# Kernel optimization log

Measured on AMD Instinct MI355X. Metric: run time of the kernel, lower is better.

Reference implementation:

```python
import jax, jax.numpy as jnp
import numpy as np

INPUT_DIM = 512
D_KQ = 64
D_V = 64
SEQ = 8192


def setup_inputs() -> dict:
    key = jax.random.key(0)
    k_x, k_q, k_k, k_v = jax.random.split(key, 4)
    x = jax.random.normal(k_x, (SEQ, INPUT_DIM), dtype=jnp.float32)
    # Original uses torch.rand (uniform [0,1)) for the parameters.
    W_query = jax.random.uniform(k_q, (INPUT_DIM, D_KQ), dtype=jnp.float32)
    W_key = jax.random.uniform(k_k, (INPUT_DIM, D_KQ), dtype=jnp.float32)
    W_value = jax.random.uniform(k_v, (INPUT_DIM, D_V), dtype=jnp.float32)
    return {"x": x, "W_query": W_query, "W_key": W_key, "W_value": W_value}


def reference(x, W_query, W_key, W_value):
    # Full-recompute path of AttentionOptimized: single-head attention.
    Q = x @ W_query          # [T, d_kq]
    K = x @ W_key            # [T, d_kq]
    V = x @ W_value          # [T, d_v]
    scale = jnp.asarray(D_KQ, x.dtype) ** 0.5
    scores = Q @ K.T         # [T, T]
    attn = jax.nn.softmax(scores / scale, axis=-1)
    return attn @ V          # [T, d_v]
```

## Files before the change

### kernel.cpp

```cpp
#include <hip/hip_runtime.h>
#include <hip/hip_bf16.h>
#include <math.h>

#define SEQ 8192
#define DIN 512
#define DH  64
#define SG  8
#define CHUNK (SEQ / SG)
#define BK  64
#define NIT (CHUNK / BK)
#define LDP 72
#define SXP 516

typedef float f32x4 __attribute__((ext_vector_type(4)));
typedef short short8 __attribute__((ext_vector_type(8)));
typedef ushort us4 __attribute__((ext_vector_type(4)));

static __device__ __forceinline__ ushort bf16_of(float v) {
  __hip_bfloat16 h = __float2bfloat16(v);
  return *reinterpret_cast<ushort*>(&h);
}
static __device__ __forceinline__ float f_of_bf16(ushort u) {
  __hip_bfloat16 h;
  *reinterpret_cast<ushort*>(&h) = u;
  return __bfloat162float(h);
}
static __device__ __forceinline__ f32x4 mfma16(short8 a, short8 b, f32x4 c) {
  return __builtin_amdgcn_mfma_f32_16x16x32_bf16(a, b, c, 0, 0, 0);
}
static __device__ __forceinline__ uint pack_bf16(float a, float b) {
  __hip_bfloat162 h2 = __float22bfloat162_rn(make_float2(a, b));
  return *reinterpret_cast<uint*>(&h2);
}

__global__ __launch_bounds__(256) void prep_kernel(
    const float* __restrict__ Wq, const float* __restrict__ Wk,
    const float* __restrict__ Wv, ushort* __restrict__ Wth,
    ushort* __restrict__ Wtl) {
  __shared__ float sw[64][65];
  const int mat = blockIdx.x >> 3;
  const int kc  = blockIdx.x & 7;
  const float* W = (mat == 0) ? Wq : ((mat == 1) ? Wk : Wv);
  const float scale = (mat == 0) ? 0.125f * 1.44269504088896f : 1.0f;
  const int tid = threadIdx.x;
#pragma unroll
  for (int j = 0; j < 16; ++j) {
    const int i = tid + 256 * j;
    sw[i >> 6][i & 63] =
        W[(size_t)(kc * 64 + (i >> 6)) * 64 + (i & 63)] * scale;
  }
  __syncthreads();
  const int n  = tid >> 2;
  const int ks = (tid & 3) * 16;
  ushort hb[16] __attribute__((aligned(16)));
  ushort lb[16] __attribute__((aligned(16)));
#pragma unroll
  for (int j = 0; j < 16; ++j) {
    const float w = sw[ks + j][n];
    const ushort h = bf16_of(w);
    hb[j] = h;
    lb[j] = bf16_of(w - f_of_bf16(h));
  }
  const size_t base = (size_t)mat * 64 * 512 + (size_t)n * 512 + kc * 64 + ks;
  *reinterpret_cast<short8*>(Wth + base)     = *reinterpret_cast<short8*>(hb);
  *reinterpret_cast<short8*>(Wth + base + 8) = *reinterpret_cast<short8*>(hb + 8);
  *reinterpret_cast<short8*>(Wtl + base)     = *reinterpret_cast<short8*>(lb);
  *reinterpret_cast<short8*>(Wtl + base + 8) = *reinterpret_cast<short8*>(lb + 8);
}

__global__ __launch_bounds__(256, 2) void pgemm_kernel(
    const float* __restrict__ x, const ushort* __restrict__ Wth,
    const ushort* __restrict__ Wtl,
    ushort* __restrict__ Qh, ushort* __restrict__ Ql,
    ushort* __restrict__ Kh, ushort* __restrict__ Kl,
    ushort* __restrict__ Vt) {
  __shared__ float sx[16][SXP];
  float* mb = &sx[0][0];

  const int tid = threadIdx.x;
  const int wv = tid >> 6, lane = tid & 63;
  const int ln = lane & 15, qd = lane >> 4;
  const int rb = blockIdx.x * 16;

  {
    const float4* xg = reinterpret_cast<const float4*>(x + (size_t)rb * DIN);
#pragma unroll
    for (int j = 0; j < 8; ++j) {
      const int idx = tid + 256 * j;
      const int row = idx >> 7;
      const int col = (idx & 127) * 4;
      *reinterpret_cast<float4*>(&sx[row][col]) = xg[idx];
    }
  }
  __syncthreads();

  f32x4 acc[3][4];
#pragma unroll
  for (int m = 0; m < 3; ++m)
#pragma unroll
    for (int nt = 0; nt < 4; ++nt)
#pragma unroll
      for (int i = 0; i < 4; ++i) acc[m][nt][i] = 0.f;

  const int kb = wv * 128;

  short8 wb[2][8];
#define LDG(kt_, m_, buf_)                                                     \
  do {                                                                         \
    const int k0_ = kb + (kt_) * 32;                                           \
    const ushort* Wh_ = Wth + (size_t)(m_) * 64 * 512;                         \
    const ushort* Wl_ = Wtl + (size_t)(m_) * 64 * 512;                         \
    _Pragma("unroll") for (int nt = 0; nt < 4; ++nt) {                         \
      const size_t wo = (size_t)(nt * 16 + ln) * 512 + k0_ + qd * 8;           \
      wb[buf_][nt * 2]     = *reinterpret_cast<const short8*>(Wh_ + wo);       \
      wb[buf_][nt * 2 + 1] = *reinterpret_cast<const short8*>(Wl_ + wo);       \
    }                                                                          \
  } while (0)

  LDG(0, 0, 0);
#pragma unroll
  for (int kt = 0; kt < 4; ++kt) {
    const int k0 = kb + kt * 32;
    float xs[8];
    *reinterpret_cast<float4*>(xs) =
        *reinterpret_cast<const float4*>(&sx[ln][k0 + qd * 8]);
    *reinterpret_cast<float4*>(xs + 4) =
        *reinterpret_cast<const float4*>(&sx[ln][k0 + qd * 8 + 4]);
    ushort ah[8] __attribute__((aligned(16)));
    ushort al[8] __attribute__((aligned(16)));
#pragma unroll
    for (int j = 0; j < 8; ++j) {
      const ushort h = bf16_of(xs[j]);
      ah[j] = h;
      al[j] = bf16_of(xs[j] - f_of_bf16(h));
    }
    const short8 Ah = *reinterpret_cast<short8*>(ah);
    const short8 Al = *reinterpret_cast<short8*>(al);
#pragma unroll
    for (int m = 0; m < 3; ++m) {
      const int g = kt * 3 + m;
      const int buf = g & 1;
      if (g < 11) {
        const int gn = g + 1;
        LDG(gn / 3, gn % 3, buf ^ 1);
      }
#pragma unroll
      for (int nt = 0; nt < 4; ++nt) {
        acc[m][nt] = mfma16(Ah, wb[buf][nt * 2],     acc[m][nt]);
        acc[m][nt] = mfma16(Ah, wb[buf][nt * 2 + 1], acc[m][nt]);
        acc[m][nt] = mfma16(Al, wb[buf][nt * 2],     acc[m][nt]);
      }
    }
  }
#undef LDG

  const int eidx = (qd * 4) * 64 + ln;
  __syncthreads();
  if (wv >= 2) {
    float* b = mb + (size_t)(wv - 2) * 3072;
#pragma unroll
    for (int m = 0; m < 3; ++m)
#pragma unroll
      for (int nt = 0; nt < 4; ++nt)
#pragma unroll
        for (int r = 0; r < 4; ++r)
          b[m * 1024 + eidx + r * 64 + nt * 16] = acc[m][nt][r];
  }
  __syncthreads();
  if (wv < 2) {
    const float* b = mb + (size_t)wv * 3072;
#pragma unroll
    for (int m = 0; m < 3; ++m)
#pragma unroll
      for (int nt = 0; nt < 4; ++nt)
#pragma unroll
        for (int r = 0; r < 4; ++r)
          acc[m][nt][r] += b[m * 1024 + eidx + r * 64 + nt * 16];
  }
  __syncthreads();
  if (wv == 1) {
#pragma unroll
    for (int m = 0; m < 3; ++m)
#pragma unroll
      for (int nt = 0; nt < 4; ++nt)
#pragma unroll
        for (int r = 0; r < 4; ++r)
          mb[m * 1024 + eidx + r * 64 + nt * 16] = acc[m][nt][r];
  }
  __syncthreads();
  if (wv == 0) {
#pragma unroll
    for (int m = 0; m < 3; ++m)
#pragma unroll
      for (int nt = 0; nt < 4; ++nt)
#pragma unroll
        for (int r = 0; r < 4; ++r)
          acc[m][nt][r] += mb[m * 1024 + eidx + r * 64 + nt * 16];

#pragma unroll
    for (int m = 0; m < 2; ++m) {
      ushort* H = (m == 0) ? Qh : Kh;
      ushort* L = (m == 0) ? Ql : Kl;
#pragma unroll
      for (int nt = 0; nt < 4; ++nt)
#pragma unroll
        for (int r = 0; r < 4; ++r) {
          const float v = acc[m][nt][r];
          const int row = rb + qd * 4 + r;
          const int col = nt * 16 + ln;
          const ushort h = bf16_of(v);
          H[(size_t)row * DH + col] = h;
          L[(size_t)row * DH + col] = bf16_of(v - f_of_bf16(h));
        }
    }
#pragma unroll
    for (int nt = 0; nt < 4; ++nt) {
      ushort vp[4] __attribute__((aligned(8)));
#pragma unroll
      for (int r = 0; r < 4; ++r) vp[r] = bf16_of(acc[2][nt][r]);
      *reinterpret_cast<us4*>(Vt + (size_t)(nt * 16 + ln) * SEQ + rb + qd * 4) =
          *reinterpret_cast<us4*>(vp);
    }
  }
}

__global__ __launch_bounds__(256, 2) void flash_kernel(
    const ushort* __restrict__ Qh, const ushort* __restrict__ Ql,
    const ushort* __restrict__ Kh, const ushort* __restrict__ Kl,
    const ushort* __restrict__ Vt,
    ushort* __restrict__ Opart, float* __restrict__ Mpart,
    float* __restrict__ Lpart) {
  __shared__ __attribute__((aligned(16))) ushort sKh[BK][LDP];
  __shared__ __attribute__((aligned(16))) ushort sKl[BK][LDP];
  __shared__ __attribute__((aligned(16))) ushort sVt[DH][LDP];

  const int tid  = threadIdx.x;
  const int wv   = tid >> 6;
  const int lane = tid & 63;
  const int ln   = lane & 15;
  const int qd   = lane >> 4;
  const int bid  = blockIdx.x;
  const int sg   = bid & 7;
  const int qt   = bid >> 3;
  const int qrow0  = qt * 128 + wv * 32;
  const int k0base = sg * CHUNK;

  const int r0 = tid >> 3, g0 = (tid & 7) * 8;
  const int r1 = r0 + 32,  g1 = g0;

  const int sA = ((qd & 1) * 2) * 16 + ln;
  const int sB = sA + 16;
  const bool hiQd = (qd >= 2);

  const ushort one_u = (ln == 0) ? (ushort)0x3F80 : (ushort)0;
  short8 afr1;
#pragma unroll
  for (int j = 0; j < 8; ++j) afr1[j] = (short)one_u;

  short8 bqh[2][2], bql[2][2];
#pragma unroll
  for (int s = 0; s < 2; ++s)
#pragma unroll
    for (int kt = 0; kt < 2; ++kt) {
      bqh[s][kt] = *reinterpret_cast<const short8*>(
          Qh + (size_t)(qrow0 + s * 16 + ln) * DH + kt * 32 + qd * 8);
      bql[s][kt] = *reinterpret_cast<const short8*>(
          Ql + (size_t)(qrow0 + s * 16 + ln) * DH + kt * 32 + qd * 8);
    }

  f32x4 accO[2][4], accL[2];
  float m_run[2] = {-INFINITY, -INFINITY};
#pragma unroll
  for (int s = 0; s < 2; ++s) {
#pragma unroll
    for (int nt = 0; nt < 4; ++nt)
#pragma unroll
      for (int i = 0; i < 4; ++i) accO[s][nt][i] = 0.f;
#pragma unroll
    for (int i = 0; i < 4; ++i) accL[s][i] = 0.f;
  }

  uint4 pk0, pk1, pl0, pl1, pv0, pv1;
#define LOAD_TILES(k0_)                                                        \
  do {                                                                         \
    pk0 = *reinterpret_cast<const uint4*>(Kh + (size_t)((k0_) + r0) * DH + g0);\
    pk1 = *reinterpret_cast<const uint4*>(Kh + (size_t)((k0_) + r1) * DH + g1);\
    pl0 = *reinterpret_cast<const uint4*>(Kl + (size_t)((k0_) + r0) * DH + g0);\
    pl1 = *reinterpret_cast<const uint4*>(Kl + (size_t)((k0_) + r1) * DH + g1);\
    pv0 = *reinterpret_cast<const uint4*>(Vt + (size_t)r0 * SEQ + (k0_) + g0); \
    pv1 = *reinterpret_cast<const uint4*>(Vt + (size_t)r1 * SEQ + (k0_) + g1); \
  } while (0)

  LOAD_TILES(k0base);

  for (int it = 0; it < NIT; ++it) {
    *reinterpret_cast<uint4*>(&sKh[r0][g0]) = pk0;
    *reinterpret_cast<uint4*>(&sKh[r1][g1]) = pk1;
    *reinterpret_cast<uint4*>(&sKl[r0][g0]) = pl0;
    *reinterpret_cast<uint4*>(&sKl[r1][g1]) = pl1;
    *reinterpret_cast<uint4*>(&sVt[r0][g0]) = pv0;
    *reinterpret_cast<uint4*>(&sVt[r1][g1]) = pv1;
    __syncthreads();

    const int k0n = k0base + ((it + 1 < NIT) ? (it + 1) : (NIT - 1)) * BK;
    LOAD_TILES(k0n);

    f32x4 accS[2][4];
#pragma unroll
    for (int nt = 0; nt < 4; ++nt) {
#pragma unroll
      for (int s = 0; s < 2; ++s)
#pragma unroll
        for (int i = 0; i < 4; ++i) accS[s][nt][i] = 0.f;
      const short8 kh0 = *reinterpret_cast<const short8*>(&sKh[nt * 16 + ln][qd * 8]);
      const short8 kh1 = *reinterpret_cast<const short8*>(&sKh[nt * 16 + ln][32 + qd * 8]);
      const short8 kl0 = *reinterpret_cast<const short8*>(&sKl[nt * 16 + ln][qd * 8]);
      const short8 kl1 = *reinterpret_cast<const short8*>(&sKl[nt * 16 + ln][32 + qd * 8]);
#pragma unroll
      for (int s = 0; s < 2; ++s) {
        accS[s][nt] = mfma16(kh0, bqh[s][0], accS[s][nt]);
        accS[s][nt] = mfma16(kh1, bqh[s][1], accS[s][nt]);
        accS[s][nt] = mfma16(kh0, bql[s][0], accS[s][nt]);
        accS[s][nt] = mfma16(kh1, bql[s][1], accS[s][nt]);
        accS[s][nt] = mfma16(kl0, bqh[s][0], accS[s][nt]);
        accS[s][nt] = mfma16(kl1, bqh[s][1], accS[s][nt]);
      }
    }

    uint pkd[2][4][2];
#pragma unroll
    for (int s = 0; s < 2; ++s) {
      float tmax = fmaxf(
          fmaxf(fmaxf(accS[s][0][0], accS[s][0][1]), fmaxf(accS[s][0][2], accS[s][0][3])),
          fmaxf(fmaxf(accS[s][1][0], accS[s][1][1]), fmaxf(accS[s][1][2], accS[s][1][3])));
      tmax = fmaxf(tmax, fmaxf(
          fmaxf(fmaxf(accS[s][2][0], accS[s][2][1]), fmaxf(accS[s][2][2], accS[s][2][3])),
          fmaxf(fmaxf(accS[s][3][0], accS[s][3][1]), fmaxf(accS[s][3][2], accS[s][3][3]))));
      tmax = fmaxf(tmax, __shfl_xor(tmax, 16));
      tmax = fmaxf(tmax, __shfl_xor(tmax, 32));
      const float mnew  = fmaxf(m_run[s], tmax);
      const float alpha = exp2f(m_run[s] - mnew);
      m_run[s] = mnew;
#pragma unroll
      for (int nt = 0; nt < 4; ++nt) {
        const float p0 = exp2f(accS[s][nt][0] - mnew);
        const float p1 = exp2f(accS[s][nt][1] - mnew);
        const float p2 = exp2f(accS[s][nt][2] - mnew);
        const float p3 = exp2f(accS[s][nt][3] - mnew);
        pkd[s][nt][0] = pack_bf16(p0, p1);
        pkd[s][nt][1] = pack_bf16(p2, p3);
#pragma unroll
        for (int i = 0; i < 4; ++i) accO[s][nt][i] *= alpha;
      }
      accL[s][0] *= alpha;
    }

#pragma unroll
    for (int kt2 = 0; kt2 < 2; ++kt2) {
      short8 pfrag[2];
#pragma unroll
      for (int s = 0; s < 2; ++s) {
        const uint pA0 = pkd[s][kt2 * 2][0],     pA1 = pkd[s][kt2 * 2][1];
        const uint pB0 = pkd[s][kt2 * 2 + 1][0], pB1 = pkd[s][kt2 * 2 + 1][1];
        uint4 du;
        const uint xA = (uint)__shfl((int)pA0, sA);
        const uint xB = (uint)__shfl((int)pB0, sA);
        du.x = hiQd ? xB : xA;
        const uint yA = (uint)__shfl((int)pA1, sA);
        const uint yB = (uint)__shfl((int)pB1, sA);
        du.y = hiQd ? yB : yA;
        const uint zA = (uint)__shfl((int)pA0, sB);
        const uint zB = (uint)__shfl((int)pB0, sB);
        du.z = hiQd ? zB : zA;
        const uint wA = (uint)__shfl((int)pA1, sB);
        const uint wB = (uint)__shfl((int)pB1, sB);
        du.w = hiQd ? wB : wA;
        pfrag[s] = *reinterpret_cast<short8*>(&du);
      }
#pragma unroll
      for (int nt2 = 0; nt2 < 4; ++nt2) {
        const short8 vA = *reinterpret_cast<const short8*>(
            &sVt[nt2 * 16 + ln][kt2 * 32 + qd * 8]);
        accO[0][nt2] = mfma16(vA, pfrag[0], accO[0][nt2]);
        accO[1][nt2] = mfma16(vA, pfrag[1], accO[1][nt2]);
      }
      accL[0] = mfma16(afr1, pfrag[0], accL[0]);
      accL[1] = mfma16(afr1, pfrag[1], accL[1]);
    }
    __syncthreads();
  }
#undef LOAD_TILES

#pragma unroll
  for (int s = 0; s < 2; ++s) {
    const int qrow = qrow0 + s * 16 + ln;
    ushort* Ob = Opart + ((size_t)sg * SEQ + qrow) * DH;
#pragma unroll
    for (int nt = 0; nt < 4; ++nt) {
      ushort op[4] __attribute__((aligned(8)));
#pragma unroll
      for (int r = 0; r < 4; ++r) op[r] = bf16_of(accO[s][nt][r]);
      *reinterpret_cast<us4*>(Ob + nt * 16 + qd * 4) =
          *reinterpret_cast<us4*>(op);
    }
    if (qd == 0) {
      Mpart[(size_t)sg * SEQ + qrow] = m_run[s];
      Lpart[(size_t)sg * SEQ + qrow] = accL[s][0];
    }
  }
}

__global__ __launch_bounds__(256) void merge_kernel(
    const ushort* __restrict__ Opart, const float* __restrict__ Mpart,
    const float* __restrict__ Lpart, float* __restrict__ out) {
  const int idx = blockIdx.x * 256 + threadIdx.x;
  const int row = idx >> 4;
  const int c4  = (idx & 15) * 4;

  float m[SG];
  float M = -INFINITY;
#pragma unroll
  for (int i = 0; i < SG; ++i) {
    m[i] = Mpart[(size_t)i * SEQ + row];
    M = fmaxf(M, m[i]);
  }
  float L = 0.f;
  float a0 = 0.f, a1 = 0.f, a2 = 0.f, a3 = 0.f;
#pragma unroll
  for (int i = 0; i < SG; ++i) {
    const float w = exp2f(m[i] - M);
    L += w * Lpart[(size_t)i * SEQ + row];
    const us4 o = *reinterpret_cast<const us4*>(
        Opart + ((size_t)i * SEQ + row) * DH + c4);
    a0 += w * f_of_bf16(o[0]);
    a1 += w * f_of_bf16(o[1]);
    a2 += w * f_of_bf16(o[2]);
    a3 += w * f_of_bf16(o[3]);
  }
  const float rL = 1.0f / L;
  float4 res = make_float4(a0 * rL, a1 * rL, a2 * rL, a3 * rL);
  *reinterpret_cast<float4*>(out + (size_t)row * DH + c4) = res;
}

extern "C" void kernel_launch(void* const* d_in, const int* in_sizes, int n_in,
                              void* d_out, int out_size, void* d_ws, size_t ws_size,
                              hipStream_t stream) {
  const float* x  = (const float*)d_in[0];
  const float* Wq = (const float*)d_in[1];
  const float* Wk = (const float*)d_in[2];
  const float* Wv = (const float*)d_in[3];
  float* out = (float*)d_out;

  const size_t S64 = (size_t)SEQ * DH;
  ushort* Qh = (ushort*)d_ws;
  ushort* Ql = Qh + S64;
  ushort* Kh = Ql + S64;
  ushort* Kl = Kh + S64;
  ushort* Vt = Kl + S64;
  ushort* Op = Vt + S64;
  ushort* Wth = Op;
  ushort* Wtl = Wth + (size_t)3 * 64 * 512;
  float*  Mp = (float*)(Op + (size_t)SG * S64);
  float*  Lp = Mp + (size_t)SG * SEQ;

  prep_kernel<<<24, 256, 0, stream>>>(Wq, Wk, Wv, Wth, Wtl);
  pgemm_kernel<<<SEQ / 16, 256, 0, stream>>>(x, Wth, Wtl, Qh, Ql, Kh, Kl, Vt);
  flash_kernel<<<(SEQ / 128) * SG, 256, 0, stream>>>(Qh, Ql, Kh, Kl, Vt, Op, Mp, Lp);
  merge_kernel<<<(SEQ * 16) / 256, 256, 0, stream>>>(Op, Mp, Lp, out);
}
```

Before: 153.2 us.

## Double-buffer K/V LDS tiles and permute K rows to remove P shuffles

Stores K/V tiles into two shared-memory buffers so each iteration needs one barrier instead of two, with the next tile written after compute. K rows are placed at permuted slots so the score accumulator layout already matches the B-operand layout for the P·V MFMA, which removes the per-iteration lane shuffles and selects. This doubles LDS use, which may reduce occupancy at two blocks per CU. It also relies on the permutation being consistent with the V column order.

```diff
diff --git a/kernel.cpp b/kernel.cpp
--- a/kernel.cpp
+++ b/kernel.cpp
@@ -31,6 +31,9 @@
 static __device__ __forceinline__ uint pack_bf16(float a, float b) {
   __hip_bfloat162 h2 = __float22bfloat162_rn(make_float2(a, b));
   return *reinterpret_cast<uint*>(&h2);
+}
+static __device__ __forceinline__ int slot_of(int p) {
+  return ((((p >> 2) & 1) * 2 + (p >> 5)) << 4) | (((p >> 3) & 3) << 2) | (p & 3);
 }
 
 __global__ __launch_bounds__(256) void prep_kernel(
@@ -230,9 +233,9 @@
     const ushort* __restrict__ Vt,
     ushort* __restrict__ Opart, float* __restrict__ Mpart,
     float* __restrict__ Lpart) {
-  __shared__ __attribute__((aligned(16))) ushort sKh[BK][LDP];
-  __shared__ __attribute__((aligned(16))) ushort sKl[BK][LDP];
-  __shared__ __attribute__((aligned(16))) ushort sVt[DH][LDP];
+  __shared__ __attribute__((aligned(16))) ushort sKh[2][BK][LDP];
+  __shared__ __attribute__((aligned(16))) ushort sKl[2][BK][LDP];
+  __shared__ __attribute__((aligned(16))) ushort sVt[2][DH][LDP];
 
   const int tid  = threadIdx.x;
   const int wv   = tid >> 6;
@@ -247,10 +250,7 @@
 
   const int r0 = tid >> 3, g0 = (tid & 7) * 8;
   const int r1 = r0 + 32,  g1 = g0;
-
-  const int sA = ((qd & 1) * 2) * 16 + ln;
-  const int sB = sA + 16;
-  const bool hiQd = (qd >= 2);
+  const int sr0 = slot_of(r0), sr1 = slot_of(r1);
 
   const ushort one_u = (ln == 0) ? (ushort)0x3F80 : (ushort)0;
   short8 afr1;
@@ -290,19 +290,23 @@
     pv0 = *reinterpret_cast<const uint4*>(Vt + (size_t)r0 * SEQ + (k0_) + g0); \
     pv1 = *reinterpret_cast<const uint4*>(Vt + (size_t)r1 * SEQ + (k0_) + g1); \
   } while (0)
+#define STORE_TILES(b_)                                                        \
+  do {                                                                         \
+    *reinterpret_cast<uint4*>(&sKh[b_][sr0][g0]) = pk0;                        \
+    *reinterpret_cast<uint4*>(&sKh[b_][sr1][g1]) = pk1;                        \
+    *reinterpret_cast<uint4*>(&sKl[b_][sr0][g0]) = pl0;                        \
+    *reinterpret_cast<uint4*>(&sKl[b_][sr1][g1]) = pl1;                        \
+    *reinterpret_cast<uint4*>(&sVt[b_][r0][g0])  = pv0;                        \
+    *reinterpret_cast<uint4*>(&sVt[b_][r1][g1])  = pv1;                        \
+  } while (0)
 
   LOAD_TILES(k0base);
+  STORE_TILES(0);
+  __syncthreads();
 
   for (int it = 0; it < NIT; ++it) {
-    *reinterpret_cast<uint4*>(&sKh[r0][g0]) = pk0;
-    *reinterpret_cast<uint4*>(&sKh[r1][g1]) = pk1;
-    *reinterpret_cast<uint4*>(&sKl[r0][g0]) = pl0;
-    *reinterpret_cast<uint4*>(&sKl[r1][g1]) = pl1;
-    *reinterpret_cast<uint4*>(&sVt[r0][g0]) = pv0;
-    *reinterpret_cast<uint4*>(&sVt[r1][g1]) = pv1;
-    __syncthreads();
-
-    const int k0n = k0base + ((it + 1 < NIT) ? (it + 1) : (NIT - 1)) * BK;
+    const int cur = it & 1;
+    const int k0n = k0base + ((it + 1 < NIT) ? (it + 1) : it) * BK;
     LOAD_TILES(k0n);
 
     f32x4 accS[2][4];
@@ -312,10 +316,10 @@
       for (int s = 0; s < 2; ++s)
 #pragma unroll
         for (int i = 0; i < 4; ++i) accS[s][nt][i] = 0.f;
-      const short8 kh0 = *reinterpret_cast<const short8*>(&sKh[nt * 16 + ln][qd * 8]);
-      const short8 kh1 = *reinterpret_cast<const short8*>(&sKh[nt * 16 + ln][32 + qd * 8]);
-      const short8 kl0 = *reinterpret_cast<const short8*>(&sKl[nt * 16 + ln][qd * 8]);
-      const short8 kl1 = *reinterpret_cast<const short8*>(&sKl[nt * 16 + ln][32 + qd * 8]);
+      const short8 kh0 = *reinterpret_cast<const short8*>(&sKh[cur][nt * 16 + ln][qd * 8]);
+      const short8 kh1 = *reinterpret_cast<const short8*>(&sKh[cur][nt * 16 + ln][32 + qd * 8]);
+      const short8 kl0 = *reinterpret_cast<const short8*>(&sKl[cur][nt * 16 + ln][qd * 8]);
+      const short8 kl1 = *reinterpret_cast<const short8*>(&sKl[cur][nt * 16 + ln][32 + qd * 8]);
 #pragma unroll
       for (int s = 0; s < 2; ++s) {
         accS[s][nt] = mfma16(kh0, bqh[s][0], accS[s][nt]);
@@ -360,36 +364,31 @@
       short8 pfrag[2];
 #pragma unroll
       for (int s = 0; s < 2; ++s) {
-        const uint pA0 = pkd[s][kt2 * 2][0],     pA1 = pkd[s][kt2 * 2][1];
-        const uint pB0 = pkd[s][kt2 * 2 + 1][0], pB1 = pkd[s][kt2 * 2 + 1][1];
         uint4 du;
-        const uint xA = (uint)__shfl((int)pA0, sA);
-        const uint xB = (uint)__shfl((int)pB0, sA);
-        du.x = hiQd ? xB : xA;
-        const uint yA = (uint)__shfl((int)pA1, sA);
-        const uint yB = (uint)__shfl((int)pB1, sA);
-        du.y = hiQd ? yB : yA;
-        const uint zA = (uint)__shfl((int)pA0, sB);
-        const uint zB = (uint)__shfl((int)pB0, sB);
-        du.z = hiQd ? zB : zA;
-        const uint wA = (uint)__shfl((int)pA1, sB);
-        const uint wB = (uint)__shfl((int)pB1, sB);
-        du.w = hiQd ? wB : wA;
+        du.x = pkd[s][kt2][0];
+        du.y = pkd[s][kt2][1];
+        du.z = pkd[s][kt2 + 2][0];
+        du.w = pkd[s][kt2 + 2][1];
         pfrag[s] = *reinterpret_cast<short8*>(&du);
       }
 #pragma unroll
       for (int nt2 = 0; nt2 < 4; ++nt2) {
         const short8 vA = *reinterpret_cast<const short8*>(
-            &sVt[nt2 * 16 + ln][kt2 * 32 + qd * 8]);
+            &sVt[cur][nt2 * 16 + ln][kt2 * 32 + qd * 8]);
         accO[0][nt2] = mfma16(vA, pfrag[0], accO[0][nt2]);
         accO[1][nt2] = mfma16(vA, pfrag[1], accO[1][nt2]);
       }
       accL[0] = mfma16(afr1, pfrag[0], accL[0]);
       accL[1] = mfma16(afr1, pfrag[1], accL[1]);
     }
-    __syncthreads();
+
+    if (it + 1 < NIT) {
+      STORE_TILES(cur ^ 1);
+      __syncthreads();
+    }
   }
 #undef LOAD_TILES
+#undef STORE_TILES
 
 #pragma unroll
   for (int s = 0; s < 2; ++s) {
```

Result: faster. 143.2 us (-6.5%).
